# Kernel optimization log

Measured on AMD Instinct MI355X. Metric: run time of the kernel, lower is better.

Reference implementation:

```python
import jax, jax.numpy as jnp
import numpy as np

B, S, D = 2, 2048, 2048
H, G = 32, 8          # num_heads, num_kv_groups
GS = H // G           # group_size = 4
HD = D // H           # head_dim = 64


def setup_inputs() -> dict:
    key = jax.random.key(0)
    ks = jax.random.split(key, 5)
    x = jax.random.normal(ks[0], (B, S, D), dtype=jnp.float32)
    Wq = jax.random.normal(ks[1], (D, D), dtype=jnp.float32) * 0.02
    Wk = jax.random.normal(ks[2], (G * HD, D), dtype=jnp.float32) * 0.02
    Wv = jax.random.normal(ks[3], (G * HD, D), dtype=jnp.float32) * 0.02
    Wo = jax.random.normal(ks[4], (D, D), dtype=jnp.float32) * 0.02
    return {"x": x, "Wq": Wq, "Wk": Wk, "Wv": Wv, "Wo": Wo}


def reference(x, Wq, Wk, Wv, Wo):
    b, s, _ = x.shape
    # Projections (nn.Linear: x @ W.T, no bias)
    # queries: view(b,s,H,HD) with head h = g*GS + j -> reshape to (b,s,G,GS,HD)
    q = (x @ Wq.T).reshape(b, s, G, GS, HD)
    k = (x @ Wk.T).reshape(b, s, G, HD)   # [b, s, G, HD]
    v = (x @ Wv.T).reshape(b, s, G, HD)
    # repeat_interleave(group_size, dim=heads): head h uses kv group h // GS,
    # which is exactly the grouped einsum below (no materialized repeat).
    scores = jnp.einsum('bqgjd,bkgd->bgjqk', q, k) / np.sqrt(HD).astype(np.float32)
    # prefill cache: ptr=0, so mask is plain causal (q_pos < k_pos masked out)
    qpos = jnp.arange(s)
    mask = qpos[:, None] < qpos[None, :]        # [s, s], True = masked
    scores = jnp.where(mask, -jnp.inf, scores)
    w = jax.nn.softmax(scores, axis=-1)         # dropout p=0.0 (eval)
    ctx = jnp.einsum('bgjqk,bkgd->bqgjd', w, v).reshape(b, s, D)
    return ctx @ Wo.T
```

## Files before the change

### kernel.cpp

```cpp
#include <hip/hip_runtime.h>
#include <hip/hip_bf16.h>

typedef unsigned short u16;
typedef short bf16x4 __attribute__((ext_vector_type(4)));
typedef short bf16x8 __attribute__((ext_vector_type(8)));
typedef float f32x4 __attribute__((ext_vector_type(4)));

#define NEG_BIG (-1e30f)
#define SCL 0.18033688f

__device__ __forceinline__ u16 f2bf(float f) {
    union { float f; unsigned int u; } x; x.f = f;
    unsigned int r = x.u + 0x7fffu + ((x.u >> 16) & 1u);
    return (u16)(r >> 16);
}

__device__ __forceinline__ unsigned cvtpk(float lo, float hi) {
    unsigned r;
    asm("v_cvt_pk_bf16_f32 %0, %1, %2" : "=v"(r) : "v"(lo), "v"(hi));
    return r;
}

__device__ __forceinline__ f32x4 mfma16(bf16x4 a, bf16x4 b, f32x4 c) {
#if __has_builtin(__builtin_amdgcn_mfma_f32_16x16x16bf16_1k)
    return __builtin_amdgcn_mfma_f32_16x16x16bf16_1k(a, b, c, 0, 0, 0);
#else
    asm("v_mfma_f32_16x16x16_bf16 %0, %1, %2, %0" : "+v"(c) : "v"(a), "v"(b));
    return c;
#endif
}

__device__ __forceinline__ void dma16(const u16* g, const u16* lds) {
    __builtin_amdgcn_global_load_lds(
        (const __attribute__((address_space(1))) unsigned int*)g,
        (__attribute__((address_space(3))) unsigned int*)lds, 16, 0, 0);
}

__device__ __forceinline__ bf16x8 sfrag(const u16* lds, int row, int kb8) {
    int slot = row * 8 + (kb8 ^ (row & 7));
    return *(const bf16x8*)(lds + slot * 8);
}

__device__ __forceinline__ bf16x4 vfrag(const u16* lds, int row, int kb, int lhi) {
    int c = kb * 2 + (lhi >> 1);
    int slot = row * 8 + (c ^ (row & 7));
    return *(const bf16x4*)(lds + slot * 8 + (lhi & 1) * 4);
}

__global__ __launch_bounds__(256) void cvt_all(const float* __restrict__ x,
                                               const float* __restrict__ wq,
                                               const float* __restrict__ wk,
                                               const float* __restrict__ wv,
                                               const float* __restrict__ wo,
                                               u16* __restrict__ xb, u16* __restrict__ wqb,
                                               u16* __restrict__ wkb, u16* __restrict__ wvb,
                                               u16* __restrict__ wob) {
    size_t i = (size_t)blockIdx.x * 256 + threadIdx.x;
    const float* s; u16* d; size_t off;
    if      (i < 1048576) { s = x;  d = xb;  off = i; }
    else if (i < 1572864) { s = wq; d = wqb; off = i - 1048576; }
    else if (i < 1703936) { s = wk; d = wkb; off = i - 1572864; }
    else if (i < 1835008) { s = wv; d = wvb; off = i - 1703936; }
    else                  { s = wo; d = wob; off = i - 1835008; }
    const float* p = s + off * 8;
    float4 a = *(const float4*)p;
    float4 b = *(const float4*)(p + 4);
    bf16x8 r;
    r[0] = (short)f2bf(a.x); r[1] = (short)f2bf(a.y);
    r[2] = (short)f2bf(a.z); r[3] = (short)f2bf(a.w);
    r[4] = (short)f2bf(b.x); r[5] = (short)f2bf(b.y);
    r[6] = (short)f2bf(b.z); r[7] = (short)f2bf(b.w);
    *(bf16x8*)(d + off * 8) = r;
}


__global__ __launch_bounds__(512, 2) void gemm_bt2(const u16* __restrict__ A,
                                                   const u16* __restrict__ Bt,
                                                   float* __restrict__ C) {
    const int K = 2048, NT = 32;
    __shared__ u16 SA[3][8192];
    __shared__ u16 SB[3][16384];
    const int t = threadIdx.x;
    const int w = t >> 6, lane = t & 63;
    const int wr = w >> 2, wc = w & 3;
    const int lhi = lane >> 4, llo = lane & 15;
    const int bid = (int)blockIdx.x;
    const int lin = (bid & 7) * 32 + (bid >> 3);
    const int by = lin & 31, bxN = lin >> 5;
    const int m0 = by * 128, n0 = bxN * 256;

    const u16* Abase = A + (size_t)m0 * K;
    const u16* Bbase = Bt + (size_t)n0 * K;

    auto STAGE = [&](int kt, int bufi) {
        const u16* Ab = Abase + kt * 64;
        const u16* Bb = Bbase + kt * 64;
        const u16* Ad = SA[bufi];
        const u16* Bd = SB[bufi];
#pragma unroll
        for (int i = 0; i < 2; ++i) {
            int s = i * 512 + t;
            int row = s >> 3, gch = (s & 7) ^ (row & 7);
            dma16(Ab + (size_t)row * K + gch * 8, Ad + (i * 512 + w * 64) * 8);
        }
#pragma unroll
        for (int i = 0; i < 4; ++i) {
            int s = i * 512 + t;
            int row = s >> 3, gch = (s & 7) ^ (row & 7);
            dma16(Bb + (size_t)row * K + gch * 8, Bd + (i * 512 + w * 64) * 8);
        }
    };

    f32x4 acc[4][4] = {};
    STAGE(0, 0);
    STAGE(1, 1);
    int cur = 0;
    for (int kt = 0; kt < NT; ++kt) {
        __builtin_amdgcn_s_barrier();
        if (kt + 2 < NT) {
            int nb = cur + 2; if (nb >= 3) nb -= 3;
            STAGE(kt + 2, nb);
            asm volatile("s_waitcnt vmcnt(12)" ::: "memory");
        } else if (kt + 1 < NT) {
            asm volatile("s_waitcnt vmcnt(6)" ::: "memory");
        } else {
            asm volatile("s_waitcnt vmcnt(0)" ::: "memory");
        }
        __builtin_amdgcn_s_barrier();
        __builtin_amdgcn_sched_barrier(0);
        const u16* Ab = SA[cur];
        const u16* Bb = SB[cur];
#pragma unroll
        for (int ks = 0; ks < 2; ++ks) {
            const int kb = ks * 4 + lhi;
            bf16x8 af[4], bfg[4];
#pragma unroll
            for (int mi = 0; mi < 4; ++mi) af[mi] = sfrag(Ab, wr * 64 + mi * 16 + llo, kb);
#pragma unroll
            for (int ni = 0; ni < 4; ++ni) bfg[ni] = sfrag(Bb, wc * 64 + ni * 16 + llo, kb);
            __builtin_amdgcn_s_setprio(1);
#pragma unroll
            for (int mi = 0; mi < 4; ++mi)
#pragma unroll
                for (int ni = 0; ni < 4; ++ni)
                    acc[mi][ni] = __builtin_amdgcn_mfma_f32_16x16x32_bf16(
                        af[mi], bfg[ni], acc[mi][ni], 0, 0, 0);
            __builtin_amdgcn_s_setprio(0);
        }
        cur = cur + 1; if (cur >= 3) cur -= 3;
    }
#pragma unroll
    for (int mi = 0; mi < 4; ++mi)
#pragma unroll
        for (int ni = 0; ni < 4; ++ni)
#pragma unroll
            for (int r = 0; r < 4; ++r) {
                int row = m0 + wr * 64 + mi * 16 + lhi * 4 + r;
                int col = n0 + wc * 64 + ni * 16 + llo;
                C[(size_t)row * 2048 + col] = acc[mi][ni][r];
            }
}

__global__ __launch_bounds__(512, 2) void gemm_qkv2(const u16* __restrict__ A,
                                                    const u16* __restrict__ Wq,
                                                    const u16* __restrict__ Wk,
                                                    const u16* __restrict__ Wv,
                                                    u16* __restrict__ Qout,
                                                    u16* __restrict__ Kout,
                                                    u16* __restrict__ Vtout) {
    const int K = 2048, NT = 32;
    __shared__ u16 SA[3][8192];
    __shared__ u16 SB[3][16384];
    const int t = threadIdx.x;
    const int w = t >> 6, lane = t & 63;
    const int wr = w >> 2, wc = w & 3;
    const int lhi = lane >> 4, llo = lane & 15;
    const int bid = (int)blockIdx.x;
    const int lin = (bid & 7) * 48 + (bid >> 3);
    const int by = lin & 31, bxN = lin >> 5;
    const int m0 = by * 128;
    const int kind = (bxN < 8) ? 0 : (bxN < 10 ? 1 : 2);
    const int n0 = (kind == 0) ? bxN * 256 : (bxN & 1) * 256;
    const u16* Bt = ((kind == 0) ? Wq : (kind == 1) ? Wk : Wv) + (size_t)n0 * K;

    const u16* Abase = A + (size_t)m0 * K;

    auto STAGE = [&](int kt, int bufi) {
        const u16* Ab = Abase + kt * 64;
        const u16* Bb = Bt + kt * 64;
        const u16* Ad = SA[bufi];
        const u16* Bd = SB[bufi];
#pragma unroll
        for (int i = 0; i < 2; ++i) {
            int s = i * 512 + t;
            int row = s >> 3, gch = (s & 7) ^ (row & 7);
            dma16(Ab + (size_t)row * K + gch * 8, Ad + (i * 512 + w * 64) * 8);
        }
#pragma unroll
        for (int i = 0; i < 4; ++i) {
            int s = i * 512 + t;
            int row = s >> 3, gch = (s & 7) ^ (row & 7);
            dma16(Bb + (size_t)row * K + gch * 8, Bd + (i * 512 + w * 64) * 8);
        }
    };

    f32x4 acc[4][4] = {};
    STAGE(0, 0);
    STAGE(1, 1);
    int cur = 0;
    for (int kt = 0; kt < NT; ++kt) {
        __builtin_amdgcn_s_barrier();
        if (kt + 2 < NT) {
            int nb = cur + 2; if (nb >= 3) nb -= 3;
            STAGE(kt + 2, nb);
            asm volatile("s_waitcnt vmcnt(12)" ::: "memory");
        } else if (kt + 1 < NT) {
            asm volatile("s_waitcnt vmcnt(6)" ::: "memory");
        } else {
            asm volatile("s_waitcnt vmcnt(0)" ::: "memory");
        }
        __builtin_amdgcn_s_barrier();
        __builtin_amdgcn_sched_barrier(0);
        const u16* Ab = SA[cur];
        const u16* Bb = SB[cur];
#pragma unroll
        for (int ks = 0; ks < 2; ++ks) {
            const int kb = ks * 4 + lhi;
            bf16x8 af[4], bfg[4];
#pragma unroll
            for (int mi = 0; mi < 4; ++mi) af[mi] = sfrag(Ab, wr * 64 + mi * 16 + llo, kb);
#pragma unroll
            for (int ni = 0; ni < 4; ++ni) bfg[ni] = sfrag(Bb, wc * 64 + ni * 16 + llo, kb);
            __builtin_amdgcn_s_setprio(1);
#pragma unroll
            for (int mi = 0; mi < 4; ++mi)
#pragma unroll
                for (int ni = 0; ni < 4; ++ni)
                    acc[mi][ni] = __builtin_amdgcn_mfma_f32_16x16x32_bf16(
                        af[mi], bfg[ni], acc[mi][ni], 0, 0, 0);
            __builtin_amdgcn_s_setprio(0);
        }
        cur = cur + 1; if (cur >= 3) cur -= 3;
    }

    if (kind == 0) {
#pragma unroll
        for (int mi = 0; mi < 4; ++mi)
#pragma unroll
            for (int ni = 0; ni < 4; ++ni)
#pragma unroll
                for (int r = 0; r < 4; ++r) {
                    int row = m0 + wr * 64 + mi * 16 + lhi * 4 + r;
                    int col = n0 + wc * 64 + ni * 16 + llo;
                    Qout[(size_t)row * 2048 + col] = f2bf(acc[mi][ni][r] * SCL);
                }
    } else if (kind == 1) {
#pragma unroll
        for (int mi = 0; mi < 4; ++mi)
#pragma unroll
            for (int ni = 0; ni < 4; ++ni)
#pragma unroll
                for (int r = 0; r < 4; ++r) {
                    int row = m0 + wr * 64 + mi * 16 + lhi * 4 + r;
                    int col = n0 + wc * 64 + ni * 16 + llo;
                    Kout[(size_t)row * 512 + col] = f2bf(acc[mi][ni][r]);
                }
    } else {
#pragma unroll
        for (int mi = 0; mi < 4; ++mi)
#pragma unroll
            for (int ni = 0; ni < 4; ++ni) {
                int row = m0 + wr * 64 + mi * 16 + lhi * 4;
                int col = n0 + wc * 64 + ni * 16 + llo;
                size_t off = ((size_t)col + (size_t)(row >> 11) * 512) * 2048 + (row & 2047);
                short4 v;
                v.x = (short)f2bf(acc[mi][ni][0]);
                v.y = (short)f2bf(acc[mi][ni][1]);
                v.z = (short)f2bf(acc[mi][ni][2]);
                v.w = (short)f2bf(acc[mi][ni][3]);
                *(short4*)(Vtout + off) = v;
            }
    }
}

__global__ __launch_bounds__(256, 4) void attn6(const u16* __restrict__ Q,
                                                const u16* __restrict__ Kbuf,
                                                const u16* __restrict__ Vtb,
                                                u16* __restrict__ Ctx) {
    __shared__ u16 Ks[2][4096];
    __shared__ u16 Vs[2][4096];
    const int bg = blockIdx.y;
    const int b = bg >> 3, g = bg & 7;
    const int t = threadIdx.x, w = t >> 6, lane = t & 63;
    const int lhi = lane >> 4, llo = lane & 15;
    const int h = g * 4 + w;
    const int wbase = w * 64;

    const u16* Kp = Kbuf + (size_t)(b * 2048) * 512 + g * 64;
    const u16* Vp = Vtb + (size_t)bg * 64 * 2048;

    const int r0 = t >> 3,          g0 = (t & 7) ^ (r0 & 7);
    const int r1 = (256 + t) >> 3,  g1 = ((256 + t) & 7) ^ (r1 & 7);

    bf16x4 ones;
    ones[0] = ones[1] = ones[2] = ones[3] = (short)0x3F80;

    auto STAGE = [&](int kt, int bufi) {
        const u16* Kt = Kp + (size_t)kt * 64 * 512;
        const u16* Vt2 = Vp + kt * 64;
        u16* Kd = Ks[bufi]; u16* Vd = Vs[bufi];
        dma16(Kt + (size_t)r0 * 512 + g0 * 8, Kd + wbase * 8);
        dma16(Vt2 + (size_t)r0 * 2048 + g0 * 8, Vd + wbase * 8);
        dma16(Kt + (size_t)r1 * 512 + g1 * 8, Kd + (256 + wbase) * 8);
        dma16(Vt2 + (size_t)r1 * 2048 + g1 * 8, Vd + (256 + wbase) * 8);
    };

#pragma unroll
    for (int ph = 0; ph < 2; ++ph) {
        const int qt = ph ? (int)blockIdx.x : 127 - (int)blockIdx.x;

        const u16* Qp = Q + ((size_t)(b * 2048 + qt * 16)) * 2048 + h * 64;
        bf16x8 aq[2];
#pragma unroll
        for (int ks = 0; ks < 2; ++ks)
            aq[ks] = *(const bf16x8*)(Qp + (size_t)llo * 2048 + ks * 32 + lhi * 8);

        f32x4 o[4] = {};
        f32x4 lac = {};
        float m_ = NEG_BIG;

        const int ktmax = (qt * 16 + 15) >> 6;

        STAGE(0, 0);
        asm volatile("s_waitcnt vmcnt(0)" ::: "memory");
        __builtin_amdgcn_s_barrier();

        for (int kt = 0; kt <= ktmax; ++kt) {
            const int cur = kt & 1;
            if (kt < ktmax) STAGE(kt + 1, cur ^ 1);
            const u16* Ksb = Ks[cur];
            const u16* Vsb = Vs[cur];

            f32x4 st[4] = {};
            __builtin_amdgcn_s_setprio(1);
#pragma unroll
            for (int ks = 0; ks < 2; ++ks) {
                const int kb8 = ks * 4 + lhi;
                bf16x8 kf[4];
#pragma unroll
                for (int kb = 0; kb < 4; ++kb) kf[kb] = sfrag(Ksb, kb * 16 + llo, kb8);
#pragma unroll
                for (int kb = 0; kb < 4; ++kb)
                    st[kb] = __builtin_amdgcn_mfma_f32_16x16x32_bf16(
                        kf[kb], aq[ks], st[kb], 0, 0, 0);
            }
            __builtin_amdgcn_s_setprio(0);

            if (kt * 64 + 63 > qt * 16) {
                int qg = qt * 16 + llo;
#pragma unroll
                for (int kb = 0; kb < 4; ++kb)
#pragma unroll
                    for (int r = 0; r < 4; ++r) {
                        int kg = kt * 64 + kb * 16 + lhi * 4 + r;
                        if (kg > qg) st[kb][r] = NEG_BIG;
                    }
            }

            float t0 = fmaxf(fmaxf(st[0][0], st[0][1]), st[0][2]);
            float t1 = fmaxf(fmaxf(st[0][3], st[1][0]), st[1][1]);
            float t2 = fmaxf(fmaxf(st[1][2], st[1][3]), st[2][0]);
            float t3 = fmaxf(fmaxf(st[2][1], st[2][2]), st[2][3]);
            float t4 = fmaxf(fmaxf(st[3][0], st[3][1]), st[3][2]);
            float mx = fmaxf(fmaxf(fmaxf(t0, t1), t2),
                             fmaxf(fmaxf(t3, t4), st[3][3]));
            mx = fmaxf(mx, __shfl_xor(mx, 16, 64));
            mx = fmaxf(mx, __shfl_xor(mx, 32, 64));

            if (__any(mx > m_ + 8.0f)) {
                float mn = fmaxf(m_, mx);
                float alpha = exp2f(m_ - mn);
                m_ = mn;
#pragma unroll
                for (int hb = 0; hb < 4; ++hb) o[hb] *= alpha;
                lac *= alpha;
            }

            bf16x4 pf[4];
#pragma unroll
            for (int kb = 0; kb < 4; ++kb) {
                float p0 = exp2f(st[kb][0] - m_);
                float p1 = exp2f(st[kb][1] - m_);
                float p2 = exp2f(st[kb][2] - m_);
                float p3 = exp2f(st[kb][3] - m_);
                union { unsigned u[2]; bf16x4 v; } pu;
                pu.u[0] = cvtpk(p0, p1);
                pu.u[1] = cvtpk(p2, p3);
                pf[kb] = pu.v;
            }

            __builtin_amdgcn_s_setprio(1);
#pragma unroll
            for (int kb = 0; kb < 4; ++kb) lac = mfma16(ones, pf[kb], lac);
#pragma unroll
            for (int kb = 0; kb < 4; ++kb)
#pragma unroll
                for (int hb = 0; hb < 4; ++hb)
                    o[hb] = mfma16(vfrag(Vsb, hb * 16 + llo, kb, lhi), pf[kb], o[hb]);
            __builtin_amdgcn_s_setprio(0);

            asm volatile("s_waitcnt vmcnt(0)" ::: "memory");
            __builtin_amdgcn_s_barrier();
        }

        float inv = 1.0f / lac[0];
        u16* Cp = Ctx + (size_t)(b * 2048 + qt * 16) * 2048 + h * 64;
#pragma unroll
        for (int hb = 0; hb < 4; ++hb) {
            union { unsigned u[2]; short4 s; } cu;
            cu.u[0] = cvtpk(o[hb][0] * inv, o[hb][1] * inv);
            cu.u[1] = cvtpk(o[hb][2] * inv, o[hb][3] * inv);
            *(short4*)(Cp + (size_t)llo * 2048 + hb * 16 + lhi * 4) = cu.s;
        }
    }
}

extern "C" void kernel_launch(void* const* d_in, const int* in_sizes, int n_in,
                              void* d_out, int out_size, void* d_ws, size_t ws_size,
                              hipStream_t stream) {
    const float* x  = (const float*)d_in[0];
    const float* Wq = (const float*)d_in[1];
    const float* Wk = (const float*)d_in[2];
    const float* Wv = (const float*)d_in[3];
    const float* Wo = (const float*)d_in[4];

    u16* xb  = (u16*)d_ws;
    u16* wqb = xb + 8388608;
    u16* wkb = wqb + 4194304;
    u16* wvb = wkb + 1048576;
    u16* wob = wvb + 1048576;
    u16* Kb  = wob + 4194304;
    u16* Vtb = Kb + 2097152;
    u16* Ctx = xb;
    u16* Qb  = (u16*)d_out;
    float* out = (float*)d_out;

    cvt_all<<<dim3(9216), 256, 0, stream>>>(x, Wq, Wk, Wv, Wo, xb, wqb, wkb, wvb, wob);
    gemm_qkv2<<<dim3(384), 512, 0, stream>>>(xb, wqb, wkb, wvb, Qb, Kb, Vtb);
    attn6<<<dim3(64, 16), 256, 0, stream>>>(Qb, Kb, Vtb, Ctx);
    gemm_bt2<<<dim3(256), 512, 0, stream>>>(Ctx, wob, out);
}
```

Before: 332.0 us.

## Restructure projection GEMMs to 256-thread blocks with larger per-wave tiles and double buffering

Both projection GEMMs move from 512-thread blocks with 128x256 tiles and a three-stage LDS pipeline to 256-thread blocks with 256x128 tiles and two-stage double buffering. Each wave now owns a 128x64 output tile (8x4 accumulators), loading fragments in quadrants to raise MFMA work per LDS read. The aim is better register-level reuse and fewer threads per tile. In exchange, occupancy drops to one block per CU, pipeline depth shrinks to two stages, and a second barrier is added per k-step, which may expose more memory latency.

```diff
diff --git a/kernel.cpp b/kernel.cpp
--- a/kernel.cpp
+++ b/kernel.cpp
@@ -74,20 +74,20 @@
 }
 
 
-__global__ __launch_bounds__(512, 2) void gemm_bt2(const u16* __restrict__ A,
+__global__ __launch_bounds__(256, 1) void gemm_bt3(const u16* __restrict__ A,
                                                    const u16* __restrict__ Bt,
                                                    float* __restrict__ C) {
     const int K = 2048, NT = 32;
-    __shared__ u16 SA[3][8192];
-    __shared__ u16 SB[3][16384];
+    __shared__ u16 SA[2][16384];
+    __shared__ u16 SB[2][8192];
     const int t = threadIdx.x;
     const int w = t >> 6, lane = t & 63;
-    const int wr = w >> 2, wc = w & 3;
+    const int wr = w >> 1, wc = w & 1;
     const int lhi = lane >> 4, llo = lane & 15;
     const int bid = (int)blockIdx.x;
     const int lin = (bid & 7) * 32 + (bid >> 3);
-    const int by = lin & 31, bxN = lin >> 5;
-    const int m0 = by * 128, n0 = bxN * 256;
+    const int bxN = lin >> 4, by = lin & 15;
+    const int m0 = by * 256, n0 = bxN * 128;
 
     const u16* Abase = A + (size_t)m0 * K;
     const u16* Bbase = Bt + (size_t)n0 * K;
@@ -98,70 +98,72 @@
         const u16* Ad = SA[bufi];
         const u16* Bd = SB[bufi];
 #pragma unroll
-        for (int i = 0; i < 2; ++i) {
-            int s = i * 512 + t;
+        for (int i = 0; i < 8; ++i) {
+            int s = i * 256 + t;
             int row = s >> 3, gch = (s & 7) ^ (row & 7);
-            dma16(Ab + (size_t)row * K + gch * 8, Ad + (i * 512 + w * 64) * 8);
+            dma16(Ab + (size_t)row * K + gch * 8, Ad + (i * 256 + w * 64) * 8);
         }
 #pragma unroll
         for (int i = 0; i < 4; ++i) {
-            int s = i * 512 + t;
+            int s = i * 256 + t;
             int row = s >> 3, gch = (s & 7) ^ (row & 7);
-            dma16(Bb + (size_t)row * K + gch * 8, Bd + (i * 512 + w * 64) * 8);
+            dma16(Bb + (size_t)row * K + gch * 8, Bd + (i * 256 + w * 64) * 8);
         }
     };
 
-    f32x4 acc[4][4] = {};
+    f32x4 acc[8][4] = {};
     STAGE(0, 0);
-    STAGE(1, 1);
-    int cur = 0;
     for (int kt = 0; kt < NT; ++kt) {
-        __builtin_amdgcn_s_barrier();
-        if (kt + 2 < NT) {
-            int nb = cur + 2; if (nb >= 3) nb -= 3;
-            STAGE(kt + 2, nb);
+        if (kt + 1 < NT) {
+            STAGE(kt + 1, (kt + 1) & 1);
             asm volatile("s_waitcnt vmcnt(12)" ::: "memory");
-        } else if (kt + 1 < NT) {
-            asm volatile("s_waitcnt vmcnt(6)" ::: "memory");
         } else {
             asm volatile("s_waitcnt vmcnt(0)" ::: "memory");
         }
         __builtin_amdgcn_s_barrier();
-        __builtin_amdgcn_sched_barrier(0);
-        const u16* Ab = SA[cur];
-        const u16* Bb = SB[cur];
-#pragma unroll
-        for (int ks = 0; ks < 2; ++ks) {
-            const int kb = ks * 4 + lhi;
-            bf16x8 af[4], bfg[4];
-#pragma unroll
-            for (int mi = 0; mi < 4; ++mi) af[mi] = sfrag(Ab, wr * 64 + mi * 16 + llo, kb);
-#pragma unroll
-            for (int ni = 0; ni < 4; ++ni) bfg[ni] = sfrag(Bb, wc * 64 + ni * 16 + llo, kb);
-            __builtin_amdgcn_s_setprio(1);
-#pragma unroll
-            for (int mi = 0; mi < 4; ++mi)
-#pragma unroll
-                for (int ni = 0; ni < 4; ++ni)
-                    acc[mi][ni] = __builtin_amdgcn_mfma_f32_16x16x32_bf16(
-                        af[mi], bfg[ni], acc[mi][ni], 0, 0, 0);
-            __builtin_amdgcn_s_setprio(0);
-        }
-        cur = cur + 1; if (cur >= 3) cur -= 3;
+        const u16* Ab = SA[kt & 1];
+        const u16* Bb = SB[kt & 1];
+#pragma unroll
+        for (int qm = 0; qm < 2; ++qm)
+#pragma unroll
+            for (int qn = 0; qn < 2; ++qn) {
+                bf16x8 af[4][2], bfg[2][2];
+#pragma unroll
+                for (int mi = 0; mi < 4; ++mi)
+#pragma unroll
+                    for (int ks = 0; ks < 2; ++ks)
+                        af[mi][ks] = sfrag(Ab, wr * 128 + qm * 64 + mi * 16 + llo, ks * 4 + lhi);
+#pragma unroll
+                for (int ni = 0; ni < 2; ++ni)
+#pragma unroll
+                    for (int ks = 0; ks < 2; ++ks)
+                        bfg[ni][ks] = sfrag(Bb, wc * 64 + qn * 32 + ni * 16 + llo, ks * 4 + lhi);
+#pragma unroll
+                for (int ks = 0; ks < 2; ++ks)
+#pragma unroll
+                    for (int mi = 0; mi < 4; ++mi)
+#pragma unroll
+                        for (int ni = 0; ni < 2; ++ni)
+                            acc[qm * 4 + mi][qn * 2 + ni] =
+                                __builtin_amdgcn_mfma_f32_16x16x32_bf16(
+                                    af[mi][ks], bfg[ni][ks],
+                                    acc[qm * 4 + mi][qn * 2 + ni], 0, 0, 0);
+            }
+        __builtin_amdgcn_s_barrier();
     }
 #pragma unroll
-    for (int mi = 0; mi < 4; ++mi)
+    for (int mi = 0; mi < 8; ++mi)
 #pragma unroll
         for (int ni = 0; ni < 4; ++ni)
 #pragma unroll
             for (int r = 0; r < 4; ++r) {
-                int row = m0 + wr * 64 + mi * 16 + lhi * 4 + r;
+                int row = m0 + wr * 128 + mi * 16 + lhi * 4 + r;
                 int col = n0 + wc * 64 + ni * 16 + llo;
                 C[(size_t)row * 2048 + col] = acc[mi][ni][r];
             }
 }
 
-__global__ __launch_bounds__(512, 2) void gemm_qkv2(const u16* __restrict__ A,
+__global__ __launch_bounds__(256, 1) void gemm_qkv3(const u16* __restrict__ A,
                                                     const u16* __restrict__ Wq,
                                                     const u16* __restrict__ Wk,
                                                     const u16* __restrict__ Wv,
@@ -169,18 +171,18 @@
                                                     u16* __restrict__ Kout,
                                                     u16* __restrict__ Vtout) {
     const int K = 2048, NT = 32;
-    __shared__ u16 SA[3][8192];
-    __shared__ u16 SB[3][16384];
+    __shared__ u16 SA[2][16384];
+    __shared__ u16 SB[2][8192];
     const int t = threadIdx.x;
     const int w = t >> 6, lane = t & 63;
-    const int wr = w >> 2, wc = w & 3;
+    const int wr = w >> 1, wc = w & 1;
     const int lhi = lane >> 4, llo = lane & 15;
     const int bid = (int)blockIdx.x;
     const int lin = (bid & 7) * 48 + (bid >> 3);
-    const int by = lin & 31, bxN = lin >> 5;
-    const int m0 = by * 128;
-    const int kind = (bxN < 8) ? 0 : (bxN < 10 ? 1 : 2);
-    const int n0 = (kind == 0) ? bxN * 256 : (bxN & 1) * 256;
+    const int bxN = lin >> 4, by = lin & 15;
+    const int m0 = by * 256;
+    const int kind = (bxN < 16) ? 0 : (bxN < 20 ? 1 : 2);
+    const int n0 = (kind == 0) ? bxN * 128 : (kind == 1) ? (bxN - 16) * 128 : (bxN - 20) * 128;
     const u16* Bt = ((kind == 0) ? Wq : (kind == 1) ? Wk : Wv) + (size_t)n0 * K;
 
     const u16* Abase = A + (size_t)m0 * K;
@@ -191,86 +193,88 @@
         const u16* Ad = SA[bufi];
         const u16* Bd = SB[bufi];
 #pragma unroll
-        for (int i = 0; i < 2; ++i) {
-            int s = i * 512 + t;
+        for (int i = 0; i < 8; ++i) {
+            int s = i * 256 + t;
             int row = s >> 3, gch = (s & 7) ^ (row & 7);
-            dma16(Ab + (size_t)row * K + gch * 8, Ad + (i * 512 + w * 64) * 8);
+            dma16(Ab + (size_t)row * K + gch * 8, Ad + (i * 256 + w * 64) * 8);
         }
 #pragma unroll
         for (int i = 0; i < 4; ++i) {
-            int s = i * 512 + t;
+            int s = i * 256 + t;
             int row = s >> 3, gch = (s & 7) ^ (row & 7);
-            dma16(Bb + (size_t)row * K + gch * 8, Bd + (i * 512 + w * 64) * 8);
+            dma16(Bb + (size_t)row * K + gch * 8, Bd + (i * 256 + w * 64) * 8);
         }
     };
 
-    f32x4 acc[4][4] = {};
+    f32x4 acc[8][4] = {};
     STAGE(0, 0);
-    STAGE(1, 1);
-    int cur = 0;
     for (int kt = 0; kt < NT; ++kt) {
-        __builtin_amdgcn_s_barrier();
-        if (kt + 2 < NT) {
-            int nb = cur + 2; if (nb >= 3) nb -= 3;
-            STAGE(kt + 2, nb);
+        if (kt + 1 < NT) {
+            STAGE(kt + 1, (kt + 1) & 1);
             asm volatile("s_waitcnt vmcnt(12)" ::: "memory");
-        } else if (kt + 1 < NT) {
-            asm volatile("s_waitcnt vmcnt(6)" ::: "memory");
         } else {
             asm volatile("s_waitcnt vmcnt(0)" ::: "memory");
         }
         __builtin_amdgcn_s_barrier();
-        __builtin_amdgcn_sched_barrier(0);
-        const u16* Ab = SA[cur];
-        const u16* Bb = SB[cur];
-#pragma unroll
-        for (int ks = 0; ks < 2; ++ks) {
-            const int kb = ks * 4 + lhi;
-            bf16x8 af[4], bfg[4];
-#pragma unroll
-            for (int mi = 0; mi < 4; ++mi) af[mi] = sfrag(Ab, wr * 64 + mi * 16 + llo, kb);
-#pragma unroll
-            for (int ni = 0; ni < 4; ++ni) bfg[ni] = sfrag(Bb, wc * 64 + ni * 16 + llo, kb);
-            __builtin_amdgcn_s_setprio(1);
-#pragma unroll
-            for (int mi = 0; mi < 4; ++mi)
-#pragma unroll
-                for (int ni = 0; ni < 4; ++ni)
-                    acc[mi][ni] = __builtin_amdgcn_mfma_f32_16x16x32_bf16(
-                        af[mi], bfg[ni], acc[mi][ni], 0, 0, 0);
-            __builtin_amdgcn_s_setprio(0);
-        }
-        cur = cur + 1; if (cur >= 3) cur -= 3;
+        const u16* Ab = SA[kt & 1];
+        const u16* Bb = SB[kt & 1];
+#pragma unroll
+        for (int qm = 0; qm < 2; ++qm)
+#pragma unroll
+            for (int qn = 0; qn < 2; ++qn) {
+                bf16x8 af[4][2], bfg[2][2];
+#pragma unroll
+                for (int mi = 0; mi < 4; ++mi)
+#pragma unroll
+                    for (int ks = 0; ks < 2; ++ks)
+                        af[mi][ks] = sfrag(Ab, wr * 128 + qm * 64 + mi * 16 + llo, ks * 4 + lhi);
+#pragma unroll
+                for (int ni = 0; ni < 2; ++ni)
+#pragma unroll
+                    for (int ks = 0; ks < 2; ++ks)
+                        bfg[ni][ks] = sfrag(Bb, wc * 64 + qn * 32 + ni * 16 + llo, ks * 4 + lhi);
+#pragma unroll
+                for (int ks = 0; ks < 2; ++ks)
+#pragma unroll
+                    for (int mi = 0; mi < 4; ++mi)
+#pragma unroll
+                        for (int ni = 0; ni < 2; ++ni)
+                            acc[qm * 4 + mi][qn * 2 + ni] =
+                                __builtin_amdgcn_mfma_f32_16x16x32_bf16(
+                                    af[mi][ks], bfg[ni][ks],
+                                    acc[qm * 4 + mi][qn * 2 + ni], 0, 0, 0);
+            }
+        __builtin_amdgcn_s_barrier();
     }
 
     if (kind == 0) {
 #pragma unroll
-        for (int mi = 0; mi < 4; ++mi)
+        for (int mi = 0; mi < 8; ++mi)
 #pragma unroll
             for (int ni = 0; ni < 4; ++ni)
 #pragma unroll
                 for (int r = 0; r < 4; ++r) {
-                    int row = m0 + wr * 64 + mi * 16 + lhi * 4 + r;
+                    int row = m0 + wr * 128 + mi * 16 + lhi * 4 + r;
                     int col = n0 + wc * 64 + ni * 16 + llo;
                     Qout[(size_t)row * 2048 + col] = f2bf(acc[mi][ni][r] * SCL);
                 }
     } else if (kind == 1) {
 #pragma unroll
-        for (int mi = 0; mi < 4; ++mi)
+        for (int mi = 0; mi < 8; ++mi)
 #pragma unroll
             for (int ni = 0; ni < 4; ++ni)
 #pragma unroll
                 for (int r = 0; r < 4; ++r) {
-                    int row = m0 + wr * 64 + mi * 16 + lhi * 4 + r;
+                    int row = m0 + wr * 128 + mi * 16 + lhi * 4 + r;
                     int col = n0 + wc * 64 + ni * 16 + llo;
                     Kout[(size_t)row * 512 + col] = f2bf(acc[mi][ni][r]);
                 }
     } else {
 #pragma unroll
-        for (int mi = 0; mi < 4; ++mi)
+        for (int mi = 0; mi < 8; ++mi)
 #pragma unroll
             for (int ni = 0; ni < 4; ++ni) {
-                int row = m0 + wr * 64 + mi * 16 + lhi * 4;
+                int row = m0 + wr * 128 + mi * 16 + lhi * 4;
                 int col = n0 + wc * 64 + ni * 16 + llo;
                 size_t off = ((size_t)col + (size_t)(row >> 11) * 512) * 2048 + (row & 2047);
                 short4 v;
@@ -446,7 +450,7 @@
     float* out = (float*)d_out;
 
     cvt_all<<<dim3(9216), 256, 0, stream>>>(x, Wq, Wk, Wv, Wo, xb, wqb, wkb, wvb, wob);
-    gemm_qkv2<<<dim3(384), 512, 0, stream>>>(xb, wqb, wkb, wvb, Qb, Kb, Vtb);
+    gemm_qkv3<<<dim3(384), 256, 0, stream>>>(xb, wqb, wkb, wvb, Qb, Kb, Vtb);
     attn6<<<dim3(64, 16), 256, 0, stream>>>(Qb, Kb, Vtb, Ctx);
-    gemm_bt2<<<dim3(256), 512, 0, stream>>>(Ctx, wob, out);
-}
+    gemm_bt3<<<dim3(256), 256, 0, stream>>>(Ctx, wob, out);
+}
```

Result: slower. 372.3 us (+12.1%).
